# Kernel tuning notes

Hardware: AMD Instinct MI355X
Metric: run time of the kernel (lower is better)

Reference implementation:

```python
import jax, jax.numpy as jnp
import numpy as np

B, T, N = 512, 1024, 48


def setup_inputs() -> dict:
    key = jax.random.key(0)
    k1, k2, k3, k4 = jax.random.split(key, 4)
    potentials = jax.random.normal(k1, (B, T, N), dtype=jnp.float32)
    y_true = jax.random.randint(k2, (B, T), 0, N, dtype=jnp.int32)
    lengths = jax.random.randint(k3, (B,), 1, T + 1, dtype=jnp.int32)
    transitions = jax.random.normal(k4, (N, N), dtype=jnp.float32)
    return {"potentials": potentials, "y_true": y_true,
            "lengths": lengths, "transitions": transitions}


def _crf_log_likelihood(potentials, tags, lengths, trans):
    # potentials: [B,T,N], tags: [B,T] int, lengths: [B] int, trans: [N,N]
    Bv, Tv, Nv = potentials.shape
    t_idx = jnp.arange(Tv)

    # ---- numerator: score of the given tag sequence ----
    unary = jnp.take_along_axis(potentials, tags[..., None], axis=2)[..., 0]  # [B,T]
    unary_mask = (t_idx[None, :] < lengths[:, None]).astype(potentials.dtype)
    unary_score = jnp.sum(unary * unary_mask, axis=1)  # [B]

    trans_scores = trans[tags[:, :-1], tags[:, 1:]]  # [B,T-1]
    pair_mask = (t_idx[None, 1:] < lengths[:, None]).astype(potentials.dtype)
    binary_score = jnp.sum(trans_scores * pair_mask, axis=1)  # [B]
    seq_score = unary_score + binary_score

    # ---- log partition: forward algorithm with length masking ----
    alpha0 = potentials[:, 0, :]  # [B,N]
    pots_rest = jnp.transpose(potentials[:, 1:, :], (1, 0, 2))  # [T-1,B,N]
    valid = (t_idx[1:, None] < lengths[None, :])  # [T-1,B]

    def step(alpha, inp):
        pot_t, v = inp  # [B,N], [B]
        # logsumexp over previous state: alpha[b,i] + trans[i,j]
        new_alpha = jax.nn.logsumexp(alpha[:, :, None] + trans[None, :, :], axis=1) + pot_t
        alpha = jnp.where(v[:, None], new_alpha, alpha)
        return alpha, None

    alpha_final, _ = jax.lax.scan(step, alpha0, (pots_rest, valid))
    log_norm = jax.nn.logsumexp(alpha_final, axis=-1)  # [B]

    return seq_score - log_norm


def reference(potentials, y_true, lengths, transitions):
    ll = _crf_log_likelihood(potentials, y_true.astype(jnp.int32),
                             lengths.astype(jnp.int32), transitions)
    return -ll  # per-sample NLL, shape [B]
```

## Files before the change

### kernel.cpp

```cpp
#include <hip/hip_runtime.h>
#include <cstdint>
#include <cstddef>

constexpr int Bb = 512;
constexpr int Tt = 1024;
constexpr int Nn = 48;
constexpr int Cc = 4;
constexpr int Lc = Tt / Cc;
constexpr int Wb = 96;

typedef float f2 __attribute__((ext_vector_type(2)));
typedef float f4 __attribute__((ext_vector_type(4)));

__device__ __forceinline__ float readlane0(float v) {
    return __int_as_float(__builtin_amdgcn_readlane(__float_as_int(v), 0));
}

__launch_bounds__(64)
__global__ void crf_nll_kernel(const float* __restrict__ pot,
                               const int*   __restrict__ ytrue,
                               const int*   __restrict__ lengths,
                               const float* __restrict__ trans,
                               float*       __restrict__ out)
{
    __shared__ __align__(16) float a_lds[64];
    __shared__ float trans_lds[Nn * Nn];

    const int b      = blockIdx.x >> 2;
    const int c      = blockIdx.x & 3;
    const int lane   = threadIdx.x;
    const int lane_c = (lane < Nn) ? lane : (Nn - 1);
    const int len    = lengths[b];

    for (int i = lane; i < Nn * Nn; i += 64) trans_lds[i] = trans[i];
    __syncthreads();

    const int start = (c == 0) ? 1 : c * Lc;
    if (c > 0 && start >= len) return;
    const int  end     = (len < (c + 1) * Lc) ? len : (c + 1) * Lc;
    const bool is_last = (end == len);

    const int*   yrow = ytrue + (size_t)b * Tt;
    const float* prow = pot + (size_t)b * Tt * Nn;

    float gold = 0.0f;
    if (c == 0) {
#pragma unroll
        for (int k = 0; k < Tt / 64; ++k) {
            const int   t    = lane + 64 * k;
            const int   yt   = yrow[t];
            const int   ytm1 = yrow[(t > 0) ? (t - 1) : 0];
            const float u    = prow[(size_t)t * Nn + yt];
            const float tr   = trans_lds[ytm1 * Nn + yt];
            const float m1   = (t < len) ? 1.0f : 0.0f;
            const float m2   = (t >= 1 && t < len) ? 1.0f : 0.0f;
            gold = fmaf(m1, u, gold);
            gold = fmaf(m2, tr, gold);
        }
    }

    f2 et2[Nn / 2];
#pragma unroll
    for (int k = 0; k < Nn / 2; ++k) {
        et2[k].x = __expf(trans_lds[(2 * k)     * Nn + lane_c]);
        et2[k].y = __expf(trans_lds[(2 * k + 1) * Nn + lane_c]);
    }

    const int   t0    = (c == 0) ? 1 : (start - Wb);
    const float pinit = prow[(size_t)(t0 - 1) * Nn + lane_c];
    const float shift = readlane0(pinit);
    float a = (lane < Nn) ? __expf(pinit - shift) : 0.0f;
    float g = (c == 0) ? shift : 0.0f;

    auto step = [&](float p, float accf) {
        a_lds[lane] = a;
        const float cc = readlane0(a);
        const float r  = __builtin_amdgcn_rcpf(cc);
        g = fmaf(accf, __logf(cc), g);
        const float f  = __expf(p) * r;

        f2 a0 = {0.0f, 0.0f}, a1 = {0.0f, 0.0f};
        f2 a2 = {0.0f, 0.0f}, a3 = {0.0f, 0.0f};
#pragma unroll
        for (int m = 0; m < 6; ++m) {
            const f4 v0 = *(const f4*)(a_lds + 8 * m);
            const f4 v1 = *(const f4*)(a_lds + 8 * m + 4);
            f2 lo0; lo0.x = v0.x; lo0.y = v0.y;
            f2 hi0; hi0.x = v0.z; hi0.y = v0.w;
            f2 lo1; lo1.x = v1.x; lo1.y = v1.y;
            f2 hi1; hi1.x = v1.z; hi1.y = v1.w;
            a0 += lo0 * et2[4 * m];
            a1 += hi0 * et2[4 * m + 1];
            a2 += lo1 * et2[4 * m + 2];
            a3 += hi1 * et2[4 * m + 3];
        }
        const f2 s2 = (a0 + a1) + (a2 + a3);
        const float s = s2.x + s2.y;
        a = s * f;
    };

    auto run = [&](int lo, int hi, float accf) {
        if (lo >= hi) return;
        float pr[8];
#pragma unroll
        for (int k = 0; k < 8; ++k) {
            int tt = lo + k; if (tt > Tt - 1) tt = Tt - 1;
            pr[k] = prow[(size_t)tt * Nn + lane_c];
        }
        int t = lo;
        while (t + 8 <= hi) {
#pragma unroll
            for (int k = 0; k < 8; ++k) {
                step(pr[k], accf);
                int tn = t + 8; if (tn > Tt - 1) tn = Tt - 1;
                pr[k] = prow[(size_t)tn * Nn + lane_c];
                ++t;
            }
        }
        float pc = prow[(size_t)((t > Tt - 1) ? (Tt - 1) : t) * Nn + lane_c];
        while (t < hi) {
            int tn = t + 1; if (tn > Tt - 1) tn = Tt - 1;
            const float pn = prow[(size_t)tn * Nn + lane_c];
            step(pc, accf);
            pc = pn;
            ++t;
        }
    };

    if (c > 0) {
        run(t0, start, 0.0f);
        g = -__logf(readlane0(a));
    }
    run(start, end, 1.0f);

    float G;
    if (is_last) {
        float se = (lane < Nn) ? a : 0.0f;
#pragma unroll
        for (int off = 32; off > 0; off >>= 1) se += __shfl_xor(se, off);
        G = g + __logf(se);
    } else {
        G = g + __logf(readlane0(a));
    }

    if (c == 0) {
        float gg = gold;
#pragma unroll
        for (int off = 32; off > 0; off >>= 1) gg += __shfl_xor(gg, off);
        G -= gg;
    }

    if (lane == 0) atomicAdd(&out[b], G);
}

extern "C" void kernel_launch(void* const* d_in, const int* in_sizes, int n_in,
                              void* d_out, int out_size, void* d_ws, size_t ws_size,
                              hipStream_t stream)
{
    const float* pot    = (const float*)d_in[0];
    const int*   ytrue  = (const int*)  d_in[1];
    const int*   lens   = (const int*)  d_in[2];
    const float* trans  = (const float*)d_in[3];
    float*       out    = (float*)d_out;

    hipMemsetAsync(out, 0, (size_t)out_size * sizeof(float), stream);
    crf_nll_kernel<<<dim3(Bb * Cc), dim3(64), 0, stream>>>(pot, ytrue, lens, trans, out);
}
```

Before: 219.3 us.

## Split sequence into 8 chunks with shorter warmup and readlane-based matvec

Doubles the number of time chunks per batch row (8 instead of 4) and shrinks the warmup window from 96 to 32 steps, so the serial recurrence per block is shorter. It also replaces the per-step LDS store/load broadcast of alpha with 48 scalar readlane operations feeding scalar FMAs. The aim is to cut serial latency and LDS round-trips, at the cost of more redundant warmup work. The shorter warmup may not converge the forward-algorithm normalisation as well, and readlanes put more work on the scalar path.

```diff
diff --git a/kernel.cpp b/kernel.cpp
--- a/kernel.cpp
+++ b/kernel.cpp
@@ -5,15 +5,12 @@
 constexpr int Bb = 512;
 constexpr int Tt = 1024;
 constexpr int Nn = 48;
-constexpr int Cc = 4;
+constexpr int Cc = 8;
 constexpr int Lc = Tt / Cc;
-constexpr int Wb = 96;
+constexpr int Wb = 32;
 
-typedef float f2 __attribute__((ext_vector_type(2)));
-typedef float f4 __attribute__((ext_vector_type(4)));
-
-__device__ __forceinline__ float readlane0(float v) {
-    return __int_as_float(__builtin_amdgcn_readlane(__float_as_int(v), 0));
+__device__ __forceinline__ float readlane_f(float v, int i) {
+    return __int_as_float(__builtin_amdgcn_readlane(__float_as_int(v), i));
 }
 
 __launch_bounds__(64)
@@ -23,11 +20,10 @@
                                const float* __restrict__ trans,
                                float*       __restrict__ out)
 {
-    __shared__ __align__(16) float a_lds[64];
     __shared__ float trans_lds[Nn * Nn];
 
-    const int b      = blockIdx.x >> 2;
-    const int c      = blockIdx.x & 3;
+    const int b      = blockIdx.x >> 3;
+    const int c      = blockIdx.x & 7;
     const int lane   = threadIdx.x;
     const int lane_c = (lane < Nn) ? lane : (Nn - 1);
     const int len    = lengths[b];
@@ -59,43 +55,37 @@
         }
     }
 
-    f2 et2[Nn / 2];
+    float et[Nn];
 #pragma unroll
-    for (int k = 0; k < Nn / 2; ++k) {
-        et2[k].x = __expf(trans_lds[(2 * k)     * Nn + lane_c]);
-        et2[k].y = __expf(trans_lds[(2 * k + 1) * Nn + lane_c]);
-    }
+    for (int i = 0; i < Nn; ++i) et[i] = __expf(trans_lds[i * Nn + lane_c]);
 
     const int   t0    = (c == 0) ? 1 : (start - Wb);
     const float pinit = prow[(size_t)(t0 - 1) * Nn + lane_c];
-    const float shift = readlane0(pinit);
+    const float shift = readlane_f(pinit, 0);
     float a = (lane < Nn) ? __expf(pinit - shift) : 0.0f;
     float g = (c == 0) ? shift : 0.0f;
 
     auto step = [&](float p, float accf) {
-        a_lds[lane] = a;
-        const float cc = readlane0(a);
+        const float cc = readlane_f(a, 0);
         const float r  = __builtin_amdgcn_rcpf(cc);
         g = fmaf(accf, __logf(cc), g);
         const float f  = __expf(p) * r;
 
-        f2 a0 = {0.0f, 0.0f}, a1 = {0.0f, 0.0f};
-        f2 a2 = {0.0f, 0.0f}, a3 = {0.0f, 0.0f};
+        float acc0 = 0.f, acc1 = 0.f, acc2 = 0.f, acc3 = 0.f;
+        float acc4 = 0.f, acc5 = 0.f, acc6 = 0.f, acc7 = 0.f;
 #pragma unroll
-        for (int m = 0; m < 6; ++m) {
-            const f4 v0 = *(const f4*)(a_lds + 8 * m);
-            const f4 v1 = *(const f4*)(a_lds + 8 * m + 4);
-            f2 lo0; lo0.x = v0.x; lo0.y = v0.y;
-            f2 hi0; hi0.x = v0.z; hi0.y = v0.w;
-            f2 lo1; lo1.x = v1.x; lo1.y = v1.y;
-            f2 hi1; hi1.x = v1.z; hi1.y = v1.w;
-            a0 += lo0 * et2[4 * m];
-            a1 += hi0 * et2[4 * m + 1];
-            a2 += lo1 * et2[4 * m + 2];
-            a3 += hi1 * et2[4 * m + 3];
+        for (int i = 0; i < Nn; i += 8) {
+            acc0 = fmaf(readlane_f(a, i + 0), et[i + 0], acc0);
+            acc1 = fmaf(readlane_f(a, i + 1), et[i + 1], acc1);
+            acc2 = fmaf(readlane_f(a, i + 2), et[i + 2], acc2);
+            acc3 = fmaf(readlane_f(a, i + 3), et[i + 3], acc3);
+            acc4 = fmaf(readlane_f(a, i + 4), et[i + 4], acc4);
+            acc5 = fmaf(readlane_f(a, i + 5), et[i + 5], acc5);
+            acc6 = fmaf(readlane_f(a, i + 6), et[i + 6], acc6);
+            acc7 = fmaf(readlane_f(a, i + 7), et[i + 7], acc7);
         }
-        const f2 s2 = (a0 + a1) + (a2 + a3);
-        const float s = s2.x + s2.y;
+        const float s = ((acc0 + acc1) + (acc2 + acc3)) +
+                        ((acc4 + acc5) + (acc6 + acc7));
         a = s * f;
     };
 
@@ -129,7 +119,7 @@
 
     if (c > 0) {
         run(t0, start, 0.0f);
-        g = -__logf(readlane0(a));
+        g = -__logf(readlane_f(a, 0));
     }
     run(start, end, 1.0f);
 
@@ -140,7 +130,7 @@
         for (int off = 32; off > 0; off >>= 1) se += __shfl_xor(se, off);
         G = g + __logf(se);
     } else {
-        G = g + __logf(readlane0(a));
+        G = g + __logf(readlane_f(a, 0));
     }
 
     if (c == 0) {
```

Result: slower. 251.4 us (+14.6%).

## Store forward-state in bf16 LDS, split sequence into 8 chunks with short warmup

Applied to the files above, without the earlier changes.

Each CRF forward-recurrence step now rounds the alpha vector to bf16 before the LDS exchange, which halves the LDS read traffic and lets each step use fewer vector loads. The accumulation is spread over eight partial sums to shorten dependency chains. The time axis is split into 8 chunks instead of 4, with the burn-in warmup cut from 96 steps to 16, which shortens the serial critical path per block and doubles the block count. The costs are a per-step bf16 rounding error that accumulates over many steps, and a much shorter warmup whose convergence to the true normalized state may be too weak, so the log-partition estimate for later chunks may lose accuracy.

```diff
diff --git a/kernel.cpp b/kernel.cpp
--- a/kernel.cpp
+++ b/kernel.cpp
@@ -5,12 +5,11 @@
 constexpr int Bb = 512;
 constexpr int Tt = 1024;
 constexpr int Nn = 48;
-constexpr int Cc = 4;
+constexpr int Cc = 8;
 constexpr int Lc = Tt / Cc;
-constexpr int Wb = 96;
+constexpr int Wb = 16;
 
 typedef float f2 __attribute__((ext_vector_type(2)));
-typedef float f4 __attribute__((ext_vector_type(4)));
 
 __device__ __forceinline__ float readlane0(float v) {
     return __int_as_float(__builtin_amdgcn_readlane(__float_as_int(v), 0));
@@ -23,11 +22,11 @@
                                const float* __restrict__ trans,
                                float*       __restrict__ out)
 {
-    __shared__ __align__(16) float a_lds[64];
+    __shared__ __align__(16) unsigned short a_bf[64];
     __shared__ float trans_lds[Nn * Nn];
 
-    const int b      = blockIdx.x >> 2;
-    const int c      = blockIdx.x & 3;
+    const int b      = blockIdx.x >> 3;
+    const int c      = blockIdx.x & 7;
     const int lane   = threadIdx.x;
     const int lane_c = (lane < Nn) ? lane : (Nn - 1);
     const int len    = lengths[b];
@@ -73,28 +72,38 @@
     float g = (c == 0) ? shift : 0.0f;
 
     auto step = [&](float p, float accf) {
-        a_lds[lane] = a;
+        const unsigned int u  = __float_as_uint(a);
+        const unsigned int rb = (u + 0x7FFFu + ((u >> 16) & 1u)) >> 16;
+        a_bf[lane] = (unsigned short)rb;
+
         const float cc = readlane0(a);
-        const float r  = __builtin_amdgcn_rcpf(cc);
+        const float rc = __builtin_amdgcn_rcpf(cc);
         g = fmaf(accf, __logf(cc), g);
-        const float f  = __expf(p) * r;
+        const float f  = __expf(p) * rc;
 
-        f2 a0 = {0.0f, 0.0f}, a1 = {0.0f, 0.0f};
-        f2 a2 = {0.0f, 0.0f}, a3 = {0.0f, 0.0f};
+        f2 acc0 = {0.f, 0.f}, acc1 = {0.f, 0.f}, acc2 = {0.f, 0.f}, acc3 = {0.f, 0.f};
+        f2 acc4 = {0.f, 0.f}, acc5 = {0.f, 0.f}, acc6 = {0.f, 0.f}, acc7 = {0.f, 0.f};
+        const uint4* ap = (const uint4*)a_bf;
 #pragma unroll
         for (int m = 0; m < 6; ++m) {
-            const f4 v0 = *(const f4*)(a_lds + 8 * m);
-            const f4 v1 = *(const f4*)(a_lds + 8 * m + 4);
-            f2 lo0; lo0.x = v0.x; lo0.y = v0.y;
-            f2 hi0; hi0.x = v0.z; hi0.y = v0.w;
-            f2 lo1; lo1.x = v1.x; lo1.y = v1.y;
-            f2 hi1; hi1.x = v1.z; hi1.y = v1.w;
-            a0 += lo0 * et2[4 * m];
-            a1 += hi0 * et2[4 * m + 1];
-            a2 += lo1 * et2[4 * m + 2];
-            a3 += hi1 * et2[4 * m + 3];
+            const uint4 v = ap[m];
+            f2 p0; p0.x = __uint_as_float(v.x << 16); p0.y = __uint_as_float(v.x & 0xFFFF0000u);
+            f2 p1; p1.x = __uint_as_float(v.y << 16); p1.y = __uint_as_float(v.y & 0xFFFF0000u);
+            f2 p2; p2.x = __uint_as_float(v.z << 16); p2.y = __uint_as_float(v.z & 0xFFFF0000u);
+            f2 p3; p3.x = __uint_as_float(v.w << 16); p3.y = __uint_as_float(v.w & 0xFFFF0000u);
+            if (m & 1) {
+                acc4 += p0 * et2[4 * m + 0];
+                acc5 += p1 * et2[4 * m + 1];
+                acc6 += p2 * et2[4 * m + 2];
+                acc7 += p3 * et2[4 * m + 3];
+            } else {
+                acc0 += p0 * et2[4 * m + 0];
+                acc1 += p1 * et2[4 * m + 1];
+                acc2 += p2 * et2[4 * m + 2];
+                acc3 += p3 * et2[4 * m + 3];
+            }
         }
-        const f2 s2 = (a0 + a1) + (a2 + a3);
+        const f2 s2 = ((acc0 + acc1) + (acc2 + acc3)) + ((acc4 + acc5) + (acc6 + acc7));
         const float s = s2.x + s2.y;
         a = s * f;
     };
```

Measured after the change: 257.1 us. 17.2% more time.
